# Kernel tuning notes

Hardware: AMD Instinct MI355X
Metric: run time of the kernel (lower is better)

## Reference

```python
import jax, jax.numpy as jnp
import numpy as np

SIGMA = 2.0


def _level(h, centers, W, b):
    # h: [n_prev, d], centers: [n_cur, d], W: [d, d] (torch Linear weight), b: [d]
    # squared distances via expansion: ||h||^2 - 2 h.c + ||c||^2  -> [n_prev, n_cur]
    sq = (jnp.sum(h * h, axis=1, keepdims=True)
          - 2.0 * (h @ centers.T)
          + jnp.sum(centers * centers, axis=1)[None, :])
    p = jax.nn.softmax(-sq / (2.0 * SIGMA), axis=1)  # softmax over centers per row
    t = jnp.tanh(h @ W.T + b)                        # [n_prev, d]
    # h_next[i] = sum_j p[j, i] * t[j]
    return p.T @ t                                   # [n_cur, d]


def setup_inputs() -> dict:
    key = jax.random.key(0)
    ks = jax.random.split(key, 11)
    d = 1024
    num_centers = [16384, 2048, 256, 32]
    inp = {"task_embedding": jax.random.normal(ks[0], (num_centers[0], d), dtype=jnp.float32)}
    # cluster centers per level (torch.rand -> uniform [0,1))
    inp["centers1"] = jax.random.uniform(ks[1], (num_centers[1], d), dtype=jnp.float32)
    inp["centers2"] = jax.random.uniform(ks[2], (num_centers[2], d), dtype=jnp.float32)
    inp["centers3"] = jax.random.uniform(ks[3], (num_centers[3], d), dtype=jnp.float32)
    # linear layers (Kaiming-uniform-ish init bound)
    bound = 1.0 / np.sqrt(d)
    for i, kw, kb in [(1, ks[4], ks[5]), (2, ks[6], ks[7]), (3, ks[8], ks[9])]:
        inp[f"W{i}"] = jax.random.uniform(kw, (d, d), minval=-bound, maxval=bound, dtype=jnp.float32)
        inp[f"b{i}"] = jax.random.uniform(kb, (d,), minval=-bound, maxval=bound, dtype=jnp.float32)
    return inp


def reference(task_embedding, centers1, centers2, centers3, W1, b1, W2, b2, W3, b3):
    h = task_embedding
    h = _level(h, centers1, W1, b1)
    h = _level(h, centers2, W2, b2)
    h = _level(h, centers3, W3, b3)
    return h
```

## Files before the change

kernel.cpp:

```cpp
#include <hip/hip_runtime.h>
#include <cmath>

typedef _Float16 half8 __attribute__((ext_vector_type(8)));
typedef _Float16 half4v __attribute__((ext_vector_type(4)));
typedef __attribute__((ext_vector_type(4))) float floatx4;

#define GLOAD_LDS16(gp, lp)                                            \
  __builtin_amdgcn_global_load_lds(                                    \
      (const __attribute__((address_space(1))) void*)(gp),             \
      (__attribute__((address_space(3))) void*)(lp), 16, 0, 0)

static inline int cdiv(int a, int b) { return (a + b - 1) / b; }

__global__ void prep(const float* __restrict__ h0, const float* __restrict__ W1,
                     const float* __restrict__ W2, const float* __restrict__ W3,
                     const float* __restrict__ c1, const float* __restrict__ c2,
                     const float* __restrict__ c3,
                     _Float16* __restrict__ hh, _Float16* __restrict__ Wh1,
                     _Float16* __restrict__ Wh2, _Float16* __restrict__ Wh3,
                     _Float16* __restrict__ cb1, _Float16* __restrict__ cb2,
                     _Float16* __restrict__ cb3,
                     float* __restrict__ cn1, float* __restrict__ cn2,
                     float* __restrict__ cn3,
                     int nh, int nw, int castBlocks, int n1, int n2) {
  int t = threadIdx.x;
  if ((int)blockIdx.x < castBlocks) {
    int gi = (blockIdx.x * 256 + t) * 4;
    const float* src; _Float16* dst; int off;
    if (gi < nh)                { src = h0; dst = hh;  off = gi; }
    else if (gi < nh + nw)      { src = W1; dst = Wh1; off = gi - nh; }
    else if (gi < nh + 2 * nw)  { src = W2; dst = Wh2; off = gi - nh - nw; }
    else if (gi < nh + 3 * nw)  { src = W3; dst = Wh3; off = gi - nh - 2 * nw; }
    else return;
    float4 v = *(const float4*)(src + off);
    half4v o = {(_Float16)v.x, (_Float16)v.y, (_Float16)v.z, (_Float16)v.w};
    *(half4v*)(dst + off) = o;
    return;
  }
  int row = blockIdx.x - castBlocks;
  const float* c; _Float16* cb; float* cn;
  if (row < n1)            { c = c1; cb = cb1; cn = cn1; }
  else if (row < n1 + n2)  { row -= n1; c = c2; cb = cb2; cn = cn2; }
  else                     { row -= n1 + n2; c = c3; cb = cb3; cn = cn3; }
  float4 v = *(const float4*)(c + (size_t)row * 1024 + t * 4);
  half4v o = {(_Float16)v.x, (_Float16)v.y, (_Float16)v.z, (_Float16)v.w};
  *(half4v*)(cb + (size_t)row * 1024 + t * 4) = o;
  float s = v.x * v.x + v.y * v.y + v.z * v.z + v.w * v.w;
  #pragma unroll
  for (int off = 32; off > 0; off >>= 1) s += __shfl_down(s, off, 64);
  __shared__ float ws[4];
  if ((t & 63) == 0) ws[t >> 6] = s;
  __syncthreads();
  if (t == 0) cn[row] = ws[0] + ws[1] + ws[2] + ws[3];
}

#define SM_CHUNK 64
__global__ void colexp_partial(_Float16* __restrict__ ST, const float* __restrict__ pmax,
                               float* __restrict__ psum, int mchunks, int ncur, int nprev) {
  int col = (blockIdx.x * 256 + threadIdx.x) * 4;
  if (col >= nprev) return;
  float m0 = -1e30f, m1 = -1e30f, m2 = -1e30f, m3 = -1e30f;
  for (int k = 0; k < mchunks; ++k) {
    float4 v = *(const float4*)(pmax + (size_t)k * nprev + col);
    m0 = fmaxf(m0, v.x); m1 = fmaxf(m1, v.y); m2 = fmaxf(m2, v.z); m3 = fmaxf(m3, v.w);
  }
  int j0 = blockIdx.y * SM_CHUNK;
  int j1 = min(j0 + SM_CHUNK, ncur);
  float s0 = 0.f, s1 = 0.f, s2 = 0.f, s3 = 0.f;
  for (int j = j0; j < j1; ++j) {
    size_t o = (size_t)j * nprev + col;
    half4v x = *(const half4v*)(ST + o);
    float e0 = __expf((float)x[0] - m0), e1 = __expf((float)x[1] - m1);
    float e2 = __expf((float)x[2] - m2), e3 = __expf((float)x[3] - m3);
    half4v e = {(_Float16)e0, (_Float16)e1, (_Float16)e2, (_Float16)e3};
    *(half4v*)(ST + o) = e;
    s0 += e0; s1 += e1; s2 += e2; s3 += e3;
  }
  float4 sv = {s0, s1, s2, s3};
  *(float4*)(psum + (size_t)blockIdx.y * nprev + col) = sv;
}

__global__ void reduce_parts(const _Float16* __restrict__ part, _Float16* __restrict__ out,
                             int mn, int S) {
  int i = (blockIdx.x * 256 + threadIdx.x) * 4;
  if (i >= mn) return;
  float a0 = 0.f, a1 = 0.f, a2 = 0.f, a3 = 0.f;
  for (int s = 0; s < S; ++s) {
    half4v v = *(const half4v*)(part + (size_t)s * mn + i);
    a0 += (float)v[0]; a1 += (float)v[1]; a2 += (float)v[2]; a3 += (float)v[3];
  }
  half4v o = {(_Float16)a0, (_Float16)a1, (_Float16)a2, (_Float16)a3};
  *(half4v*)(out + i) = o;
}

enum { EP_LOGIT = 0, EP_TANH = 1, EP_TANHP = 2, EP_F16 = 3, EP_F32 = 4, EP_PART = 5 };

template<int BM, int BN, int EPI>
__launch_bounds__(256, 4)
__global__ void gemm_nt(const _Float16* __restrict__ A,
                        const _Float16* __restrict__ B,
                        void* __restrict__ Cout,
                        const float* __restrict__ aux1,
                        const float* __restrict__ aux2,
                        float* __restrict__ pmax,
                        int pnchunks,
                        int M, int N, int K, int kLen) {
  constexpr int BK = 64;
  constexpr int WTM = BM / 2, WTN = BN / 2;
  constexpr int FM = WTM / 16, FN = WTN / 16;
  __shared__ __align__(16) _Float16 As[BM * BK];
  __shared__ __align__(16) _Float16 Bs[BN * BK];
  float* smf = (float*)As;
  const int tid  = threadIdx.x;
  const int lane = tid & 63;
  const int wave = tid >> 6;
  const int wm = wave >> 1, wn = wave & 1;
  const int mBase = blockIdx.x * BM, nBase = blockIdx.y * BN;
  const int kBase = blockIdx.z * kLen;
  const int lr    = lane & 15;
  const int kHalf = (lane >> 4) << 3;

  const int srOff  = lane >> 3;
  const int schunk = (lane & 7) ^ srOff;
  floatx4 acc[FM][FN] = {};
  constexpr int AV = BM * BK / (256 * 8);
  constexpr int BV = BN * BK / (256 * 8);

  for (int k0 = kBase; k0 < kBase + kLen; k0 += BK) {
    #pragma unroll
    for (int v = 0; v < AV; ++v) {
      int rowBase = v * 32 + wave * 8;
      int gm = mBase + rowBase + srOff;
      if (gm >= M) gm = M - 1;
      GLOAD_LDS16(A + (size_t)gm * K + k0 + schunk * 8, &As[rowBase * BK]);
    }
    #pragma unroll
    for (int v = 0; v < BV; ++v) {
      int rowBase = v * 32 + wave * 8;
      int gn = nBase + rowBase + srOff;
      if (gn >= N) gn = N - 1;
      GLOAD_LDS16(B + (size_t)gn * K + k0 + schunk * 8, &Bs[rowBase * BK]);
    }
    __syncthreads();
    #pragma unroll
    for (int kk = 0; kk < BK; kk += 32) {
      const int q = (kk + kHalf) >> 3;
      half8 af[FM], bfv[FN];
      #pragma unroll
      for (int i = 0; i < FM; ++i) {
        int r = wm * WTM + i * 16 + lr;
        af[i] = *(const half8*)(&As[r * BK + ((q ^ (r & 7)) << 3)]);
      }
      #pragma unroll
      for (int j = 0; j < FN; ++j) {
        int r = wn * WTN + j * 16 + lr;
        bfv[j] = *(const half8*)(&Bs[r * BK + ((q ^ (r & 7)) << 3)]);
      }
      #pragma unroll
      for (int i = 0; i < FM; ++i)
        #pragma unroll
        for (int j = 0; j < FN; ++j)
          acc[i][j] = __builtin_amdgcn_mfma_f32_16x16x32_f16(af[i], bfv[j], acc[i][j], 0, 0, 0);
    }
    __syncthreads();
  }

  if (EPI == EP_TANH) {
    if (tid < BN) {
      int col = nBase + tid;
      float ssum = 0.f;
      if (col < N)
        for (int k = 0; k < pnchunks; ++k) ssum += aux2[(size_t)k * N + col];
      smf[tid] = 1.f / ssum;
    }
    __syncthreads();
  }

  const int rBase = (lane >> 4) << 2;
  float lmax[FN];
  #pragma unroll
  for (int j = 0; j < FN; ++j) lmax[j] = -1e30f;
  #pragma unroll
  for (int i = 0; i < FM; ++i) {
    #pragma unroll
    for (int j = 0; j < FN; ++j) {
      #pragma unroll
      for (int r = 0; r < 4; ++r) {
        int row = mBase + wm * WTM + i * 16 + rBase + r;
        int col = nBase + wn * WTN + j * 16 + lr;
        if (row < M && col < N) {
          float v = acc[i][j][r];
          size_t o = (size_t)row * N + col;
          if (EPI == EP_LOGIT) {
            v = 0.5f * v - 0.25f * aux1[row];
            ((_Float16*)Cout)[o] = (_Float16)v;
            lmax[j] = fmaxf(lmax[j], v);
          } else if (EPI == EP_TANH) {
            v = tanhf(v + aux1[row]) * smf[col - nBase];
            ((_Float16*)Cout)[o] = (_Float16)v;
          } else if (EPI == EP_TANHP) {
            v = tanhf(v + aux1[row]);
            ((_Float16*)Cout)[o] = (_Float16)v;
          } else if (EPI == EP_F16) {
            ((_Float16*)Cout)[o] = (_Float16)v;
          } else if (EPI == EP_PART) {
            ((_Float16*)Cout)[(size_t)blockIdx.z * M * N + o] = (_Float16)v;
          } else {
            ((float*)Cout)[o] = v;
          }
        }
      }
    }
  }
  if (EPI == EP_LOGIT) {
    #pragma unroll
    for (int j = 0; j < FN; ++j) {
      float m = lmax[j];
      m = fmaxf(m, __shfl_xor(m, 16, 64));
      m = fmaxf(m, __shfl_xor(m, 32, 64));
      if ((lane >> 4) == 0) smf[wm * BN + wn * WTN + j * 16 + lr] = m;
    }
    __syncthreads();
    if (tid < BN) {
      int col = nBase + tid;
      if (col < N)
        pmax[(size_t)blockIdx.x * N + col] = fmaxf(smf[tid], smf[BN + tid]);
    }
  }
}

#define BAR8 __builtin_amdgcn_s_barrier()
#define LGKM0 asm volatile("s_waitcnt lgkmcnt(0)" ::: "memory")
#define VMC(n) asm volatile("s_waitcnt vmcnt(" #n ")" ::: "memory")
#define STG_A(b, kk, h)                                                              \
  do {                                                                               \
    GLOAD_LDS16(gA + (size_t)((h) * 128) * K + (kk),                                 \
                &As[b][((h) * 128 + wave * 8) * 64]);                                \
    GLOAD_LDS16(gA + (size_t)((h) * 128 + 64) * K + (kk),                            \
                &As[b][((h) * 128 + 64 + wave * 8) * 64]);                           \
  } while (0)
#define STG_B(b, kk, h)                                                              \
  do {                                                                               \
    GLOAD_LDS16(gB + (size_t)((h) * 128) * K + (kk),                                 \
                &Bs[b][((h) * 128 + wave * 8) * 64]);                                \
    GLOAD_LDS16(gB + (size_t)((h) * 128 + 64) * K + (kk),                            \
                &Bs[b][((h) * 128 + 64 + wave * 8) * 64]);                           \
  } while (0)
#define LDA8(s, base)                                                                \
  { _Pragma("unroll") for (int i_ = 0; i_ < 8; ++i_)                                 \
      af[s][i_] = *(const half8*)((base) + aoff + i_ * 1024 + ((s) ? xr1 : xr0)); }
#define LDB2(s, j0, base)                                                            \
  { bf[s][(j0)] = *(const half8*)((base) + boff + (j0) * 1024 + ((s) ? xr1 : xr0));  \
    bf[s][(j0) + 1] =                                                                \
        *(const half8*)((base) + boff + ((j0) + 1) * 1024 + ((s) ? xr1 : xr0)); }
#define MF16(s, nh)                                                                  \
  { __builtin_amdgcn_s_setprio(1);                                                   \
    _Pragma("unroll") for (int i_ = 0; i_ < 8; ++i_) {                               \
      acc[i_][2 * (nh)] = __builtin_amdgcn_mfma_f32_16x16x32_f16(                    \
          af[s][i_], bf[s][2 * (nh)], acc[i_][2 * (nh)], 0, 0, 0);                   \
      acc[i_][2 * (nh) + 1] = __builtin_amdgcn_mfma_f32_16x16x32_f16(                \
          af[s][i_], bf[s][2 * (nh) + 1], acc[i_][2 * (nh) + 1], 0, 0, 0);           \
    }                                                                                \
    __builtin_amdgcn_s_setprio(0); }

template<int EPI>
__launch_bounds__(512, 2)
__global__ void gemm8(const _Float16* __restrict__ A, const _Float16* __restrict__ B,
                      void* __restrict__ Cout, const float* __restrict__ aux1,
                      const float* __restrict__ aux2, float* __restrict__ pmax,
                      int pnchunks, int M, int N, int K, int kLen) {
  __shared__ __align__(16) _Float16 As[2][256 * 64];
  __shared__ __align__(16) _Float16 Bs[2][256 * 64];
  float* smf = (float*)&As[0][0];
  const int tid  = threadIdx.x;
  const int lane = tid & 63;
  const int wave = tid >> 6;
  const int wm = wave >> 2, wn = wave & 3;
  const int mBase = blockIdx.x * 256, nBase = blockIdx.y * 256;
  const int kBase = blockIdx.z * kLen;
  const int lr = lane & 15;
  const int xr0 = (((lane >> 4) ^ (lr & 7)) << 3);
  const int xr1 = ((((lane >> 4) + 4) ^ (lr & 7)) << 3);
  const int aoff = (wm * 128 + lr) * 64;
  const int boff = (wn * 64 + lr) * 64;
  const int srOff = lane >> 3;
  const int sch8 = ((lane & 7) ^ srOff) << 3;
  const _Float16* gA = A + (size_t)(mBase + wave * 8 + srOff) * K + kBase + sch8;
  const _Float16* gB = B + (size_t)(nBase + wave * 8 + srOff) * K + kBase + sch8;
  const _Float16* As0 = &As[0][0];
  const _Float16* As1 = &As[1][0];
  const _Float16* Bs0 = &Bs[0][0];
  const _Float16* Bs1 = &Bs[1][0];

  half8 af[2][8], bf[2][4];
  floatx4 acc[8][4] = {};
  const int NT = kLen / 64;

  STG_A(0, 0, 0); STG_A(0, 0, 1); STG_B(0, 0, 0); STG_B(0, 0, 1);
  STG_A(1, 64, 0); STG_A(1, 64, 1); STG_B(1, 64, 0);
  VMC(6);
  BAR8;
  LDA8(0, As0);
  LDB2(0, 0, Bs0);

  int kc = 0;
  for (int t = 0; t + 3 < NT; t += 2, kc += 128) {
    LDB2(0, 2, Bs0);  STG_B(1, kc + 64, 1);
    BAR8; LGKM0; MF16(0, 0); BAR8;
    LDA8(1, As0);  LDB2(1, 0, Bs0);
    BAR8; LGKM0; MF16(0, 1); BAR8;
    LDB2(1, 2, Bs0);  STG_A(0, kc + 128, 0);  VMC(2);
    BAR8; LGKM0; MF16(1, 0); BAR8;
    LDA8(0, As1);  LDB2(0, 0, Bs1);  STG_A(0, kc + 128, 1);  STG_B(0, kc + 128, 0);
    BAR8; LGKM0; MF16(1, 1); BAR8;
    LDB2(0, 2, Bs1);  STG_B(0, kc + 128, 1);
    BAR8; LGKM0; MF16(0, 0); BAR8;
    LDA8(1, As1);  LDB2(1, 0, Bs1);
    BAR8; LGKM0; MF16(0, 1); BAR8;
    LDB2(1, 2, Bs1);  STG_A(1, kc + 192, 0);  VMC(2);
    BAR8; LGKM0; MF16(1, 0); BAR8;
    LDA8(0, As0);  LDB2(0, 0, Bs0);  STG_A(1, kc + 192, 1);  STG_B(1, kc + 192, 0);
    BAR8; LGKM0; MF16(1, 1); BAR8;
  }
  LDB2(0, 2, Bs0);  STG_B(1, kc + 64, 1);
  BAR8; LGKM0; MF16(0, 0); BAR8;
  LDA8(1, As0);  LDB2(1, 0, Bs0);
  BAR8; LGKM0; MF16(0, 1); BAR8;
  LDB2(1, 2, Bs0);  VMC(0);
  BAR8; LGKM0; MF16(1, 0); BAR8;
  LDA8(0, As1);  LDB2(0, 0, Bs1);
  BAR8; LGKM0; MF16(1, 1); BAR8;
  LDB2(0, 2, Bs1);
  BAR8; LGKM0; MF16(0, 0); BAR8;
  LDA8(1, As1);  LDB2(1, 0, Bs1);
  BAR8; LGKM0; MF16(0, 1); BAR8;
  LDB2(1, 2, Bs1);
  BAR8; LGKM0; MF16(1, 0); BAR8;
  MF16(1, 1);
  __syncthreads();

  if (EPI == EP_TANH) {
    if (tid < 256) {
      int col = nBase + tid;
      float ssum = 0.f;
      for (int k = 0; k < pnchunks; ++k) ssum += aux2[(size_t)k * N + col];
      smf[tid] = 1.f / ssum;
    }
    __syncthreads();
  }

  const int rBase = (lane >> 4) << 2;
  float lmax[4];
  #pragma unroll
  for (int j = 0; j < 4; ++j) lmax[j] = -1e30f;
  #pragma unroll
  for (int i = 0; i < 8; ++i)
    #pragma unroll
    for (int j = 0; j < 4; ++j)
      #pragma unroll
      for (int r = 0; r < 4; ++r) {
        int row = mBase + wm * 128 + i * 16 + rBase + r;
        int col = nBase + wn * 64 + j * 16 + lr;
        float v = acc[i][j][r];
        size_t o = (size_t)row * N + col;
        if (EPI == EP_LOGIT) {
          v = 0.5f * v - 0.25f * aux1[row];
          ((_Float16*)Cout)[o] = (_Float16)v;
          lmax[j] = fmaxf(lmax[j], v);
        } else if (EPI == EP_TANH) {
          v = tanhf(v + aux1[row]) * smf[col - nBase];
          ((_Float16*)Cout)[o] = (_Float16)v;
        } else {
          ((_Float16*)Cout)[(size_t)blockIdx.z * M * N + o] = (_Float16)v;
        }
      }
  if (EPI == EP_LOGIT) {
    #pragma unroll
    for (int j = 0; j < 4; ++j) {
      float m2 = lmax[j];
      m2 = fmaxf(m2, __shfl_xor(m2, 16, 64));
      m2 = fmaxf(m2, __shfl_xor(m2, 32, 64));
      if ((lane >> 4) == 0) smf[wm * 256 + wn * 64 + j * 16 + lr] = m2;
    }
    __syncthreads();
    if (tid < 256) {
      int col = nBase + tid;
      pmax[(size_t)blockIdx.x * N + col] = fmaxf(smf[tid], smf[256 + tid]);
    }
  }
}
#undef BAR8
#undef LGKM0
#undef VMC
#undef STG_A
#undef STG_B
#undef LDA8
#undef LDB2
#undef MF16

template<int EPI>
static int launch_gemm(int M, int N, int K, const _Float16* A, const _Float16* B,
                       void* C, const float* a1, const float* a2, float* pmax,
                       int pnchunks, hipStream_t s) {
  long b128   = (long)cdiv(M, 128) * cdiv(N, 128);
  long b12864 = (long)cdiv(M, 128) * cdiv(N, 64);
  if (b128 >= 192) {
    gemm_nt<128, 128, EPI><<<dim3(cdiv(M, 128), cdiv(N, 128)), 256, 0, s>>>(
        A, B, C, a1, a2, pmax, pnchunks, M, N, K, K);
    return 128;
  } else if (M >= 128 && b12864 >= 192) {
    gemm_nt<128, 64, EPI><<<dim3(cdiv(M, 128), cdiv(N, 64)), 256, 0, s>>>(
        A, B, C, a1, a2, pmax, pnchunks, M, N, K, K);
    return 128;
  } else {
    gemm_nt<64, 64, EPI><<<dim3(cdiv(M, 64), cdiv(N, 64)), 256, 0, s>>>(
        A, B, C, a1, a2, pmax, pnchunks, M, N, K, K);
    return 64;
  }
}

static void launch_gemm_splitk(int M, int N, int K, int S,
                               const _Float16* A, const _Float16* B,
                               _Float16* Cpart, _Float16* Cout, hipStream_t s) {
  int kLen = K / S;
  long b128 = (long)cdiv(M, 128) * cdiv(N, 128) * S;
  if (M >= 128 && N >= 128 && b128 >= 256) {
    gemm_nt<128, 128, EP_PART><<<dim3(cdiv(M, 128), cdiv(N, 128), S), 256, 0, s>>>(
        A, B, Cpart, nullptr, nullptr, nullptr, 0, M, N, K, kLen);
  } else {
    gemm_nt<64, 64, EP_PART><<<dim3(cdiv(M, 64), cdiv(N, 64), S), 256, 0, s>>>(
        A, B, Cpart, nullptr, nullptr, nullptr, 0, M, N, K, kLen);
  }
  int mn = M * N;
  reduce_parts<<<cdiv(mn, 1024), 256, 0, s>>>(Cpart, Cout, mn, S);
}

template<int BM, int BN>
__launch_bounds__(256, 2)
__global__ void fused_ls(const _Float16* __restrict__ A,
                         const _Float16* __restrict__ B,
                         _Float16* __restrict__ Eout,
                         const float* __restrict__ cn,
                         int M, int N, int K) {
  constexpr int BK = 64;
  constexpr int WTM = BM / 2, WTN = BN / 2;
  constexpr int FM = WTM / 16, FN = WTN / 16;
  constexpr int TLD = BN + 4;
  constexpr int STAGE_B = (BM + BN) * BK * 2;
  constexpr int TILE_B  = BM * TLD * 4;
  constexpr int SM_B = STAGE_B > TILE_B ? STAGE_B : TILE_B;
  __shared__ __align__(16) char smem[SM_B];
  _Float16* As = (_Float16*)smem;
  _Float16* Bs = As + BM * BK;
  float* tile = (float*)smem;
  __shared__ float redm[256], reds[256];
  const int tid  = threadIdx.x;
  const int lane = tid & 63;
  const int wave = tid >> 6;
  const int wm = wave >> 1, wn = wave & 1;
  const int nBase = blockIdx.x * BN;
  const int lr    = lane & 15;
  const int kHalf = (lane >> 4) << 3;
  const int srOff  = lane >> 3;
  const int schunk = (lane & 7) ^ srOff;
  floatx4 acc[FM][FN] = {};
  constexpr int AV = BM * BK / (256 * 8);
  constexpr int BV = BN * BK / (256 * 8);

  for (int k0 = 0; k0 < K; k0 += BK) {
    #pragma unroll
    for (int v = 0; v < AV; ++v) {
      int rowBase = v * 32 + wave * 8;
      GLOAD_LDS16(A + (size_t)(rowBase + srOff) * K + k0 + schunk * 8, &As[rowBase * BK]);
    }
    #pragma unroll
    for (int v = 0; v < BV; ++v) {
      int rowBase = v * 32 + wave * 8;
      GLOAD_LDS16(B + (size_t)(nBase + rowBase + srOff) * K + k0 + schunk * 8, &Bs[rowBase * BK]);
    }
    __syncthreads();
    #pragma unroll
    for (int kk = 0; kk < BK; kk += 32) {
      const int q = (kk + kHalf) >> 3;
      half8 af[FM], bfv[FN];
      #pragma unroll
      for (int i = 0; i < FM; ++i) {
        int r = wm * WTM + i * 16 + lr;
        af[i] = *(const half8*)(&As[r * BK + ((q ^ (r & 7)) << 3)]);
      }
      #pragma unroll
      for (int j = 0; j < FN; ++j) {
        int r = wn * WTN + j * 16 + lr;
        bfv[j] = *(const half8*)(&Bs[r * BK + ((q ^ (r & 7)) << 3)]);
      }
      #pragma unroll
      for (int i = 0; i < FM; ++i)
        #pragma unroll
        for (int j = 0; j < FN; ++j)
          acc[i][j] = __builtin_amdgcn_mfma_f32_16x16x32_f16(af[i], bfv[j], acc[i][j], 0, 0, 0);
    }
    __syncthreads();
  }

  const int rBase = (lane >> 4) << 2;
  #pragma unroll
  for (int i = 0; i < FM; ++i)
    #pragma unroll
    for (int j = 0; j < FN; ++j)
      #pragma unroll
      for (int r = 0; r < 4; ++r) {
        int row = wm * WTM + i * 16 + rBase + r;
        int col = wn * WTN + j * 16 + lr;
        tile[row * TLD + col] = 0.5f * acc[i][j][r] - 0.25f * cn[row];
      }
  __syncthreads();

  constexpr int P = 256 / BN;
  const int c = tid & (BN - 1);
  const int p = tid / BN;
  float m = -1e30f;
  for (int j = p; j < M; j += P) m = fmaxf(m, tile[j * TLD + c]);
  redm[p * BN + c] = m;
  __syncthreads();
  float mf = redm[c];
  #pragma unroll
  for (int q = 1; q < P; ++q) mf = fmaxf(mf, redm[q * BN + c]);
  float s = 0.f;
  for (int j = p; j < M; j += P) {
    float e = __expf(tile[j * TLD + c] - mf);
    tile[j * TLD + c] = e;
    s += e;
  }
  reds[p * BN + c] = s;
  __syncthreads();
  float l = 0.f;
  #pragma unroll
  for (int q = 0; q < P; ++q) l += reds[q * BN + c];
  const float li = 1.f / l;
  for (int j = p; j < M; j += P)
    Eout[(size_t)j * N + nBase + c] = (_Float16)(tile[j * TLD + c] * li);
}

extern "C" void kernel_launch(void* const* d_in, const int* in_sizes, int n_in,
                              void* d_out, int out_size, void* d_ws, size_t ws_size,
                              hipStream_t stream) {
  const float* h0 = (const float*)d_in[0];
  const float* c1 = (const float*)d_in[1];
  const float* c2 = (const float*)d_in[2];
  const float* c3 = (const float*)d_in[3];
  const float* W1 = (const float*)d_in[4];
  const float* b1 = (const float*)d_in[5];
  const float* W2 = (const float*)d_in[6];
  const float* b2 = (const float*)d_in[7];
  const float* W3 = (const float*)d_in[8];
  const float* b3 = (const float*)d_in[9];

  const int d = 1024;
  const int N0 = 16384, N1 = 2048, N2 = 256, N3 = 32;

  char* w = (char*)d_ws;
  size_t off = 0;
  auto alloc = [&](size_t bytes) {
    void* p = w + off;
    off += (bytes + 255) & ~(size_t)255;
    return p;
  };
  _Float16* hb  = (_Float16*)alloc((size_t)N0 * d * 2);
  _Float16* cb1 = (_Float16*)alloc((size_t)N1 * d * 2);
  _Float16* cb2 = (_Float16*)alloc((size_t)N2 * d * 2);
  _Float16* cb3 = (_Float16*)alloc((size_t)N3 * d * 2);
  float* cn1 = (float*)alloc((size_t)N1 * 4);
  float* cn2 = (float*)alloc((size_t)N2 * 4);
  float* cn3 = (float*)alloc((size_t)N3 * 4);
  _Float16* Wb1 = (_Float16*)alloc((size_t)d * d * 2);
  _Float16* Wb2 = (_Float16*)alloc((size_t)d * d * 2);
  _Float16* Wb3 = (_Float16*)alloc((size_t)d * d * 2);
  _Float16* ST = (_Float16*)alloc((size_t)N1 * N0 * 2);
  _Float16* tT = (_Float16*)alloc((size_t)d * N0 * 2);
  float* pmax = (float*)alloc((size_t)32 * N0 * 4);
  float* psum = (float*)alloc((size_t)32 * N0 * 4);
  _Float16* h1b = (_Float16*)alloc((size_t)N1 * d * 2);
  _Float16* h2b = (_Float16*)alloc((size_t)N2 * d * 2);
  _Float16* Cpart = (_Float16*)alloc((size_t)8 * N1 * d * 2);
  _Float16* E = ST;
  (void)ws_size; (void)in_sizes; (void)n_in; (void)out_size;

  int nh = N0 * d, nw = d * d;
  int castBlocks = cdiv(nh + 3 * nw, 1024);
  prep<<<castBlocks + N1 + N2 + N3, 256, 0, stream>>>(
      h0, W1, W2, W3, c1, c2, c3, hb, Wb1, Wb2, Wb3, cb1, cb2, cb3,
      cn1, cn2, cn3, nh, nw, castBlocks, N1, N2);

  gemm8<EP_LOGIT><<<dim3(N1 / 256, N0 / 256), 512, 0, stream>>>(
      cb1, hb, ST, cn1, nullptr, pmax, 0, N1, N0, d, d);
  colexp_partial<<<dim3(N0 / 1024, cdiv(N1, SM_CHUNK)), 256, 0, stream>>>(
      ST, pmax, psum, N1 / 256, N1, N0);
  gemm8<EP_TANH><<<dim3(d / 256, N0 / 256), 512, 0, stream>>>(
      Wb1, hb, tT, b1, psum, nullptr, cdiv(N1, SM_CHUNK), d, N0, d, d);
  gemm8<EP_PART><<<dim3(N1 / 256, d / 256, 8), 512, 0, stream>>>(
      E, tT, Cpart, nullptr, nullptr, nullptr, 0, N1, d, N0, N0 / 8);
  reduce_parts<<<cdiv(N1 * d, 1024), 256, 0, stream>>>(Cpart, h1b, N1 * d, 8);

  fused_ls<256, 64><<<N1 / 64, 256, 0, stream>>>(cb2, h1b, E, cn2, N2, N1, d);
  launch_gemm<EP_TANHP>(d, N1, d, Wb2, h1b, tT, b2, nullptr, nullptr, 0, stream);
  launch_gemm_splitk(N2, d, N1, 8, E, tT, Cpart, h2b, stream);

  fused_ls<32, 64><<<N2 / 64, 256, 0, stream>>>(cb3, h2b, E, cn3, N3, N2, d);
  launch_gemm<EP_TANHP>(d, N2, d, Wb3, h2b, tT, b3, nullptr, nullptr, 0, stream);
  launch_gemm<EP_F32>(N3, d, N2, E, tT, d_out, nullptr, nullptr, nullptr, 0, stream);
}
```

Before: 522.9 us.

## Add XCD-aware block swizzle and rebalance gemm8 global-to-LDS prefetch schedule

Remaps the linear workgroup index so consecutive tiles land on the same XCD, aiming to improve L2 reuse of shared A/B panels in both GEMM kernels. The pmax writes now use the remapped bx. The gemm8 main loop is also reordered: B's second half is staged with the rest of the prologue, and A and B stages are grouped into pairs. The vmcnt waits move to after the MFMA block so global loads overlap more compute. This adds risk around LDS buffer hazards if the new wait placement is not strictly correct.

```diff
diff --git a/kernel.cpp b/kernel.cpp
--- a/kernel.cpp
+++ b/kernel.cpp
@@ -93,6 +93,14 @@
   *(half4v*)(out + i) = o;
 }
 
+#define XCD_SWZ(BMv, BNv)                                                       \
+  const int gx_ = gridDim.x;                                                    \
+  const int nwg_ = gx_ * gridDim.y;                                             \
+  int lin_ = blockIdx.y * gx_ + blockIdx.x;                                     \
+  if ((nwg_ & 7) == 0) lin_ = (lin_ & 7) * (nwg_ >> 3) + (lin_ >> 3);           \
+  const int bx = lin_ % gx_, by = lin_ / gx_;                                   \
+  const int mBase = bx * (BMv), nBase = by * (BNv);
+
 enum { EP_LOGIT = 0, EP_TANH = 1, EP_TANHP = 2, EP_F16 = 3, EP_F32 = 4, EP_PART = 5 };
 
 template<int BM, int BN, int EPI>
@@ -115,7 +123,7 @@
   const int lane = tid & 63;
   const int wave = tid >> 6;
   const int wm = wave >> 1, wn = wave & 1;
-  const int mBase = blockIdx.x * BM, nBase = blockIdx.y * BN;
+  XCD_SWZ(BM, BN)
   const int kBase = blockIdx.z * kLen;
   const int lr    = lane & 15;
   const int kHalf = (lane >> 4) << 3;
@@ -224,7 +232,7 @@
     if (tid < BN) {
       int col = nBase + tid;
       if (col < N)
-        pmax[(size_t)blockIdx.x * N + col] = fmaxf(smf[tid], smf[BN + tid]);
+        pmax[(size_t)bx * N + col] = fmaxf(smf[tid], smf[BN + tid]);
     }
   }
 }
@@ -276,7 +284,7 @@
   const int lane = tid & 63;
   const int wave = tid >> 6;
   const int wm = wave >> 2, wn = wave & 3;
-  const int mBase = blockIdx.x * 256, nBase = blockIdx.y * 256;
+  XCD_SWZ(256, 256)
   const int kBase = blockIdx.z * kLen;
   const int lr = lane & 15;
   const int xr0 = (((lane >> 4) ^ (lr & 7)) << 3);
@@ -297,37 +305,37 @@
   const int NT = kLen / 64;
 
   STG_A(0, 0, 0); STG_A(0, 0, 1); STG_B(0, 0, 0); STG_B(0, 0, 1);
-  STG_A(1, 64, 0); STG_A(1, 64, 1); STG_B(1, 64, 0);
-  VMC(6);
+  STG_A(1, 64, 0); STG_A(1, 64, 1); STG_B(1, 64, 0); STG_B(1, 64, 1);
+  VMC(8);
   BAR8;
   LDA8(0, As0);
   LDB2(0, 0, Bs0);
 
   int kc = 0;
   for (int t = 0; t + 3 < NT; t += 2, kc += 128) {
-    LDB2(0, 2, Bs0);  STG_B(1, kc + 64, 1);
+    LDB2(0, 2, Bs0);
     BAR8; LGKM0; MF16(0, 0); BAR8;
     LDA8(1, As0);  LDB2(1, 0, Bs0);
     BAR8; LGKM0; MF16(0, 1); BAR8;
-    LDB2(1, 2, Bs0);  STG_A(0, kc + 128, 0);  VMC(2);
-    BAR8; LGKM0; MF16(1, 0); BAR8;
-    LDA8(0, As1);  LDB2(0, 0, Bs1);  STG_A(0, kc + 128, 1);  STG_B(0, kc + 128, 0);
+    LDB2(1, 2, Bs0);  STG_A(0, kc + 128, 0);  STG_A(0, kc + 128, 1);
+    BAR8; LGKM0; MF16(1, 0); VMC(4); BAR8;
+    LDA8(0, As1);  LDB2(0, 0, Bs1);  STG_B(0, kc + 128, 0);  STG_B(0, kc + 128, 1);
     BAR8; LGKM0; MF16(1, 1); BAR8;
-    LDB2(0, 2, Bs1);  STG_B(0, kc + 128, 1);
+    LDB2(0, 2, Bs1);
     BAR8; LGKM0; MF16(0, 0); BAR8;
     LDA8(1, As1);  LDB2(1, 0, Bs1);
     BAR8; LGKM0; MF16(0, 1); BAR8;
-    LDB2(1, 2, Bs1);  STG_A(1, kc + 192, 0);  VMC(2);
-    BAR8; LGKM0; MF16(1, 0); BAR8;
-    LDA8(0, As0);  LDB2(0, 0, Bs0);  STG_A(1, kc + 192, 1);  STG_B(1, kc + 192, 0);
+    LDB2(1, 2, Bs1);  STG_A(1, kc + 192, 0);  STG_A(1, kc + 192, 1);
+    BAR8; LGKM0; MF16(1, 0); VMC(4); BAR8;
+    LDA8(0, As0);  LDB2(0, 0, Bs0);  STG_B(1, kc + 192, 0);  STG_B(1, kc + 192, 1);
     BAR8; LGKM0; MF16(1, 1); BAR8;
   }
-  LDB2(0, 2, Bs0);  STG_B(1, kc + 64, 1);
+  LDB2(0, 2, Bs0);
   BAR8; LGKM0; MF16(0, 0); BAR8;
   LDA8(1, As0);  LDB2(1, 0, Bs0);
   BAR8; LGKM0; MF16(0, 1); BAR8;
-  LDB2(1, 2, Bs0);  VMC(0);
-  BAR8; LGKM0; MF16(1, 0); BAR8;
+  LDB2(1, 2, Bs0);
+  BAR8; LGKM0; MF16(1, 0); VMC(0); BAR8;
   LDA8(0, As1);  LDB2(0, 0, Bs1);
   BAR8; LGKM0; MF16(1, 1); BAR8;
   LDB2(0, 2, Bs1);
@@ -385,7 +393,7 @@
     __syncthreads();
     if (tid < 256) {
       int col = nBase + tid;
-      pmax[(size_t)blockIdx.x * N + col] = fmaxf(smf[tid], smf[256 + tid]);
+      pmax[(size_t)bx * N + col] = fmaxf(smf[tid], smf[256 + tid]);
     }
   }
 }
```

Result: no change. 528.9 us (+1.2%).
